# Performance work log

Measured on AMD Instinct MI355X. Metric: run time of the kernel, lower is better.

## Reference

```python
import jax, jax.numpy as jnp
import numpy as np

EMB = 128  # embedding_size hard-coded in source
NW = 8192  # weak samples
NS = 8192  # strong samples
FD = 1024  # encoder input feature dim
QN = 1024  # queue max_size
C = 80     # num classes (COCO-style WSOD)


def setup_inputs() -> dict:
    key = jax.random.key(0)
    ks = jax.random.split(key, 9)
    return {
        "feats_strong": jax.random.normal(ks[0], (NS, FD), jnp.float32),
        "feats_weak": jax.random.normal(ks[1], (NW, FD), jnp.float32),
        "strong_labels": jax.random.randint(ks[2], (NS,), 0, C, jnp.int64),
        "weak_labels": jax.random.randint(ks[3], (NW,), 0, C, jnp.int64),
        "Wq": jax.random.normal(ks[4], (FD, EMB), jnp.float32) * (FD ** -0.5),
        "bq": jax.random.normal(ks[5], (EMB,), jnp.float32) * 0.01,
        "Wk": jax.random.normal(ks[6], (FD, EMB), jnp.float32) * (FD ** -0.5),
        "bk": jax.random.normal(ks[7], (EMB,), jnp.float32) * 0.01,
        "queue": jax.random.normal(ks[8], (QN, EMB), jnp.float32),
    }


def reference(feats_strong, feats_weak, strong_labels, weak_labels, Wq, bq, Wk, bk, queue):
    # Encoders applied to all samples at once (original loops one-by-one).
    q_all = feats_weak @ Wq + bq            # [NW, EMB]
    k_all = feats_strong @ Wk + bk          # [NS, EMB]
    k_all = jax.lax.stop_gradient(k_all)    # k = k.detach() in source

    w, s = weak_labels, strong_labels
    eq_ws = w[:, None] == s[None, :]                      # [NW, NS] weak-vs-strong label match
    cnt = eq_ws.astype(jnp.int32).sum(1)                  # num_strong per weak sample
    valid = cnt > 0                                       # `if weak_label in strong_labels`

    # rank of i among weak indices with the same label (position in torch.where output)
    eq_ww = (w[:, None] == w[None, :]).astype(jnp.int32)
    rank = jnp.tril(eq_ww, -1).sum(1)                     # [NW]
    sel = rank % jnp.maximum(cnt, 1)                      # `% num_strong`

    # occurrence rank of each strong index within its label group
    eq_ss = (s[:, None] == s[None, :]).astype(jnp.int32)
    occ = jnp.tril(eq_ss, -1).sum(1)                      # [NS]

    # index_strong[i] = sel[i]-th strong index whose label == w[i]
    M = eq_ws & (occ[None, :] == sel[:, None])            # [NW, NS]
    idx = jnp.argmax(M, axis=1)                           # [NW]

    q = q_all                                             # [NW, EMB]
    k = k_all[idx]                                        # [NW, EMB]

    l_pos = jnp.sum(q * k, axis=-1, keepdims=True)        # bmm([N,1,E],[N,E,1]) -> [N,1]
    l_neg = q @ queue.reshape(EMB, -1)                    # queue.view(EMB, -1): row-major reshape
    logits = jnp.concatenate([l_pos, l_neg], axis=1)      # [NW, 1+QN]

    # CrossEntropy with target 0 on each valid row, mean over valid rows
    ce = -jax.nn.log_softmax(logits, axis=-1)[:, 0]
    m = valid.astype(logits.dtype)
    loss = jnp.sum(ce * m) / jnp.maximum(m.sum(), 1.0)
    return loss
```

## Files before the change

### kernel.cpp

```cpp
#include <hip/hip_runtime.h>
#include <hip/hip_bf16.h>

#define NW   8192
#define NS   8192
#define FD   1024
#define EMB  128
#define QN   1024
#define NC   80

typedef unsigned short ushort_t;
typedef unsigned int   uint_t;
typedef __attribute__((ext_vector_type(8))) short short8;
typedef __attribute__((ext_vector_type(4))) float f32x4;

#define OFF_Q      0u
#define OFF_K      1048576u
#define OFF_WTQ    2097152u
#define OFF_WTK    2129920u
#define OFF_HIST   2752512u
#define OFF_RANK   2752640u
#define OFF_CNT    2760832u
#define OFF_BHS    2785408u
#define OFF_BHW    2787968u
#define OFF_ACC    2790528u
#define OFF_QT     2790532u
#define OFF_TABLE  3000000u

__device__ __forceinline__ ushort_t f2bf(float f) {
    uint_t u = __float_as_uint(f);
    u = (u + 0x7fffu + ((u >> 16) & 1u)) >> 16;
    return (ushort_t)u;
}
__device__ __forceinline__ uint_t pack2(float a, float b) {
    return (uint_t)f2bf(a) | ((uint_t)f2bf(b) << 16);
}

#define GLOAD_LDS16(gp, lp)                                                     \
    __builtin_amdgcn_global_load_lds(                                           \
        (const __attribute__((address_space(1))) void*)(gp),                    \
        (__attribute__((address_space(3))) void*)(lp), 16, 0, 0)

__global__ __launch_bounds__(256) void cvtbh_k(const float* __restrict__ Wq,
                                               const float* __restrict__ Wk,
                                               const float* __restrict__ queue,
                                               const int* __restrict__ s_lab,
                                               const int* __restrict__ w_lab,
                                               ushort_t* __restrict__ Wtq,
                                               ushort_t* __restrict__ Wtk,
                                               ushort_t* __restrict__ Qt,
                                               int* __restrict__ bhs,
                                               int* __restrict__ bhw,
                                               float* __restrict__ accum,
                                               int* __restrict__ counter) {
    int bx = blockIdx.x;
    int t = threadIdx.x;
    if (bx >= 384) {
        __shared__ int h[NC];
        int b2 = bx - 384, z = b2 >> 5, cb = b2 & 31;
        const int* lab = z ? w_lab : s_lab;
        int* bh = z ? bhw : bhs;
        if (t < NC) h[t] = 0;
        __syncthreads();
        atomicAdd(&h[lab[cb * 256 + t]], 1);
        __syncthreads();
        if (t < NC) bh[cb * NC + t] = h[t];
        return;
    }
    __shared__ float tile[32][33];
    int z = bx >> 7, flat = bx & 127;
    if (z == 0 && flat == 0) {
        if (t < 2) accum[t] = 0.0f;
        if (t == 2) *counter = 0;
    }
    const float* in; ushort_t* out; int r0, c0, C;
    if (z < 2) { in = z ? Wk : Wq; out = z ? Wtk : Wtq; C = 128;
                 r0 = (flat >> 2) * 32; c0 = (flat & 3) * 32; }
    else       { in = queue; out = Qt; C = 1024;
                 r0 = (flat & 3) * 32; c0 = (flat >> 2) * 32; }
    int i = t >> 3, j0 = (t & 7) * 4;
    float4 v = *(const float4*)(in + (size_t)(r0 + i) * C + c0 + j0);
    tile[i][j0] = v.x; tile[i][j0 + 1] = v.y; tile[i][j0 + 2] = v.z; tile[i][j0 + 3] = v.w;
    __syncthreads();
    uint2 pk;
    pk.x = pack2(tile[j0][i], tile[j0 + 1][i]);
    pk.y = pack2(tile[j0 + 2][i], tile[j0 + 3][i]);
    size_t oaddr;
    int k0 = r0 + j0, n = c0 + i;
    if (z < 2) {
        oaddr = (size_t)(k0 >> 6) * 8192 + (size_t)((k0 >> 3) & 7) * 1024
              + (size_t)n * 8 + (k0 & 7);
    } else {
        int c = k0 >> 3;
        oaddr = ((size_t)n * 16 + (c ^ (n & 15))) * 8 + (k0 & 7);
    }
    *(uint2*)(out + oaddr) = pk;
}

__global__ __launch_bounds__(256) void enc_mfma_k(const float* __restrict__ A0,
                                                  const float* __restrict__ A1,
                                                  const ushort_t* __restrict__ Wt0,
                                                  const ushort_t* __restrict__ Wt1,
                                                  const float* __restrict__ b0_,
                                                  const float* __restrict__ b1_,
                                                  float* __restrict__ out0,
                                                  float* __restrict__ out1,
                                                  const int* __restrict__ s_lab,
                                                  const int* __restrict__ w_lab,
                                                  const int* __restrict__ bhs,
                                                  const int* __restrict__ bhw,
                                                  int* __restrict__ table,
                                                  int* __restrict__ rank,
                                                  int* __restrict__ hist) {
    __shared__ __align__(16) char smem[73728];

    int bx = blockIdx.x;
    int t = threadIdx.x;

    if (bx < 64) {
        int* ll = (int*)smem;
        int b2 = bx, z = b2 >> 5, cb = b2 & 31;
        const int* lab = z ? w_lab : s_lab;
        const int* bh = z ? bhw : bhs;
        int j = cb * 256 + t;
        int c = lab[j];
        ll[t] = c;
        __syncthreads();
        int r = 0;
        for (int b = 0; b < cb; b++) r += bh[b * NC + c];
        for (int jj = 0; jj < t; jj++) r += (ll[jj] == c) ? 1 : 0;
        if (z) rank[j] = r;
        else   table[c * 8192 + r] = j;
        if (b2 == 0 && t < 128) {
            int h = 0;
            if (t < NC)
                for (int b = 0; b < 32; b++) h += bhs[b * NC + t];
            hist[t] = h;
        }
        return;
    }

    int bxg = bx - 64;
    int which = bxg >> 8;
    int mtile = bxg & 255;
    const float*    A    = which ? A1 : A0;
    const ushort_t* Wt   = which ? Wt1 : Wt0;
    const float*    bias = which ? b1_ : b0_;
    float*          out  = which ? out1 : out0;
    int row0 = mtile * 32;

    int wv = t >> 6, ln = t & 63;
    int wm = wv >> 1, wn = wv & 1;
    int lane15 = ln & 15, kg = ln >> 4;

    int ar0 = wv * 8 + (ln >> 4);
    int ar1 = ar0 + 4;
    const float* gA0 = A + (size_t)(row0 + ar0) * FD + (((ln & 15) ^ (ar0 & 15))) * 4;
    const float* gA1 = A + (size_t)(row0 + ar1) * FD + (((ln & 15) ^ (ar1 & 15))) * 4;
    const ushort_t* gB = Wt + (size_t)wv * 2048 + ln * 8;

    f32x4 acc[4];
#pragma unroll
    for (int nt = 0; nt < 4; nt++) acc[nt] = (f32x4){0.f, 0.f, 0.f, 0.f};

#define STAGE(BUF, KB)                                                           \
    { char* sb = smem + (BUF) * 24576;                                           \
      GLOAD_LDS16(gA0 + (size_t)(KB) * 64, sb + wv * 2048);                      \
      GLOAD_LDS16(gA1 + (size_t)(KB) * 64, sb + wv * 2048 + 1024);               \
      const ushort_t* gb = gB + (size_t)(KB) * 8192;                             \
      char* bb = sb + 8192 + wv * 4096;                                          \
      GLOAD_LDS16(gb,        bb);                                                \
      GLOAD_LDS16(gb + 512,  bb + 1024);                                         \
      GLOAD_LDS16(gb + 1024, bb + 2048);                                         \
      GLOAD_LDS16(gb + 1536, bb + 3072); }

#define K2_ITER(KB, CURB, STB, VMSTR)                                            \
    { asm volatile("s_waitcnt vmcnt(" VMSTR ")" ::: "memory");                   \
      __builtin_amdgcn_s_barrier();                                              \
      __builtin_amdgcn_sched_barrier(0);                                         \
      if ((KB) < 14) STAGE(STB, (KB) + 2)                                        \
      { char* lb = smem + (CURB) * 24576;                                        \
        _Pragma("unroll")                                                        \
        for (int ks = 0; ks < 2; ks++) {                                         \
            int r_l = wm * 16 + lane15;                                          \
            int c0 = ks * 8 + kg * 2;                                            \
            float4 alo = *(const float4*)(lb + ((size_t)r_l * 16 + ((c0)     ^ (r_l & 15))) * 16); \
            float4 ahi = *(const float4*)(lb + ((size_t)r_l * 16 + ((c0 + 1) ^ (r_l & 15))) * 16); \
            uint4 pk;                                                            \
            pk.x = pack2(alo.x, alo.y); pk.y = pack2(alo.z, alo.w);              \
            pk.z = pack2(ahi.x, ahi.y); pk.w = pack2(ahi.z, ahi.w);              \
            short8 af = __builtin_bit_cast(short8, pk);                          \
            int kgg = ks * 4 + kg;                                               \
            _Pragma("unroll")                                                    \
            for (int nt = 0; nt < 4; nt++) {                                     \
                uint4 bv = *(const uint4*)(lb + 8192 +                           \
                            ((size_t)kgg * 128 + wn * 64 + nt * 16 + lane15) * 16); \
                acc[nt] = __builtin_amdgcn_mfma_f32_16x16x32_bf16(               \
                    af, __builtin_bit_cast(short8, bv), acc[nt], 0, 0, 0);       \
            }                                                                    \
        } }                                                                      \
    }

    STAGE(0, 0)
    STAGE(1, 1)
#pragma unroll 1
    for (int kb3 = 0; kb3 < 15; kb3 += 3) {
        K2_ITER(kb3 + 0, 0, 2, "6")
        K2_ITER(kb3 + 1, 1, 0, "6")
        K2_ITER(kb3 + 2, 2, 1, "6")
    }
    K2_ITER(15, 0, 0, "0")
#undef K2_ITER
#undef STAGE

#pragma unroll
    for (int nt = 0; nt < 4; nt++) {
        int col = wn * 64 + nt * 16 + lane15;
        float bv = bias[col];
        int rbase = row0 + wm * 16 + kg * 4;
#pragma unroll
        for (int j = 0; j < 4; j++)
            out[(size_t)(rbase + j) * EMB + col] = acc[nt][j] + bv;
    }
}

__global__ __launch_bounds__(256) void ce_mfma_k(const float* __restrict__ q,
                                                 const float* __restrict__ k,
                                                 const ushort_t* __restrict__ Qt,
                                                 const int* __restrict__ rank,
                                                 const int* __restrict__ table,
                                                 const int* __restrict__ w,
                                                 const int* __restrict__ hist,
                                                 float* __restrict__ accum,
                                                 int* __restrict__ counter,
                                                 float* __restrict__ outp) {
    __shared__ int   idx_lds[16];
    __shared__ float lpos_lds[16];
    __shared__ float mg[4][16][2];
    int t = threadIdx.x;
    int r0 = blockIdx.x * 16;

    if (t < 16) {
        int i = r0 + t;
        int c = w[i];
        int cc = hist[c];
        idx_lds[t] = (cc > 0) ? table[c * 8192 + (rank[i] % cc)] : 0;
    }
    __syncthreads();

    {
        int rr = t >> 4;
        int o = (t & 15) * 8;
        const float4* qa = (const float4*)(q + (size_t)(r0 + rr) * EMB + o);
        const float4* ka = (const float4*)(k + (size_t)idx_lds[rr] * EMB + o);
        float4 a0 = qa[0], b0 = ka[0], a1 = qa[1], b1 = ka[1];
        float s = a0.x * b0.x + a0.y * b0.y + a0.z * b0.z + a0.w * b0.w
                + a1.x * b1.x + a1.y * b1.y + a1.z * b1.z + a1.w * b1.w;
        s += __shfl_xor(s, 1); s += __shfl_xor(s, 2);
        s += __shfl_xor(s, 4); s += __shfl_xor(s, 8);
        if ((t & 15) == 0) lpos_lds[rr] = s;
    }

    int wv = t >> 6, ln = t & 63;
    int lane15 = ln & 15, kg = ln >> 4;

    short8 afr[4];
#pragma unroll
    for (int ks = 0; ks < 4; ks++) {
        const float4* p = (const float4*)(q + (size_t)(r0 + lane15) * EMB + ks * 32 + kg * 8);
        float4 a = p[0], b = p[1];
        uint4 pk;
        pk.x = pack2(a.x, a.y); pk.y = pack2(a.z, a.w);
        pk.z = pack2(b.x, b.y); pk.w = pack2(b.z, b.w);
        afr[ks] = __builtin_bit_cast(short8, pk);
    }

    f32x4 acc[16];
#pragma unroll
    for (int nc = 0; nc < 16; nc++) acc[nc] = (f32x4){0.f, 0.f, 0.f, 0.f};

#pragma unroll
    for (int nc = 0; nc < 16; nc++) {
        int n_g = nc * 64 + wv * 16 + lane15;
        const ushort_t* bp = Qt + (size_t)n_g * 128;
#pragma unroll
        for (int ks = 0; ks < 4; ks++) {
            int c = ks * 4 + kg;
            uint4 bb = *(const uint4*)(bp + (size_t)(c ^ lane15) * 8);
            acc[nc] = __builtin_amdgcn_mfma_f32_16x16x32_bf16(
                afr[ks], __builtin_bit_cast(short8, bb), acc[nc], 0, 0, 0);
        }
    }

#pragma unroll
    for (int j = 0; j < 4; j++) {
        float mx = -1e30f;
#pragma unroll
        for (int nc = 0; nc < 16; nc++) mx = fmaxf(mx, acc[nc][j]);
        mx = fmaxf(mx, __shfl_xor(mx, 1));
        mx = fmaxf(mx, __shfl_xor(mx, 2));
        mx = fmaxf(mx, __shfl_xor(mx, 4));
        mx = fmaxf(mx, __shfl_xor(mx, 8));
        float s = 0.f;
#pragma unroll
        for (int nc = 0; nc < 16; nc++) s += __expf(acc[nc][j] - mx);
        s += __shfl_xor(s, 1);
        s += __shfl_xor(s, 2);
        s += __shfl_xor(s, 4);
        s += __shfl_xor(s, 8);
        if (lane15 == 0) {
            mg[wv][kg * 4 + j][0] = mx;
            mg[wv][kg * 4 + j][1] = s;
        }
    }
    __syncthreads();
    if (wv == 0) {
        float cv = 0.f, cc = 0.f;
        if (t < 16) {
            int i = r0 + t;
            float m0 = mg[0][t][0], l0 = mg[0][t][1];
            float m1 = mg[1][t][0], l1 = mg[1][t][1];
            float m2 = mg[2][t][0], l2 = mg[2][t][1];
            float m3 = mg[3][t][0], l3 = mg[3][t][1];
            float lp = lpos_lds[t];
            float m = fmaxf(fmaxf(fmaxf(m0, m1), fmaxf(m2, m3)), lp);
            float l = l0 * __expf(m0 - m) + l1 * __expf(m1 - m)
                    + l2 * __expf(m2 - m) + l3 * __expf(m3 - m) + __expf(lp - m);
            float ce = -(lp - m - __logf(l));
            if (hist[w[i]] > 0) { cv = ce; cc = 1.f; }
        }
        cv += __shfl_xor(cv, 1);  cc += __shfl_xor(cc, 1);
        cv += __shfl_xor(cv, 2);  cc += __shfl_xor(cc, 2);
        cv += __shfl_xor(cv, 4);  cc += __shfl_xor(cc, 4);
        cv += __shfl_xor(cv, 8);  cc += __shfl_xor(cc, 8);
        if (t == 0) {
            atomicAdd(&accum[0], cv);
            atomicAdd(&accum[1], cc);
            __threadfence();
            int done = atomicAdd(counter, 1);
            if (done == 511) {
                float s = atomicAdd(&accum[0], 0.0f);
                float c = atomicAdd(&accum[1], 0.0f);
                outp[0] = s / fmaxf(c, 1.0f);
            }
        }
    }
}

extern "C" void kernel_launch(void* const* d_in, const int* in_sizes, int n_in,
                              void* d_out, int out_size, void* d_ws, size_t ws_size,
                              hipStream_t stream) {
    const float* feats_strong = (const float*)d_in[0];
    const float* feats_weak   = (const float*)d_in[1];
    const int*   s_lab        = (const int*)d_in[2];
    const int*   w_lab        = (const int*)d_in[3];
    const float* Wq           = (const float*)d_in[4];
    const float* bq           = (const float*)d_in[5];
    const float* Wk           = (const float*)d_in[6];
    const float* bk           = (const float*)d_in[7];
    const float* queue        = (const float*)d_in[8];

    float*    wsf = (float*)d_ws;
    int*      wsi = (int*)d_ws;

    float*    q_g   = wsf + OFF_Q;
    float*    k_g   = wsf + OFF_K;
    int*      table = wsi + OFF_TABLE;
    ushort_t* Wtq   = (ushort_t*)(wsi + OFF_WTQ);
    ushort_t* Wtk   = (ushort_t*)(wsi + OFF_WTK);
    int*      hist  = wsi + OFF_HIST;
    int*      rank  = wsi + OFF_RANK;
    int*      cnt   = wsi + OFF_CNT;
    int*      bhs   = wsi + OFF_BHS;
    int*      bhw   = wsi + OFF_BHW;
    float*    accum = wsf + OFF_ACC;
    ushort_t* Qt    = (ushort_t*)(wsi + OFF_QT);

    cvtbh_k<<<448, 256, 0, stream>>>(Wq, Wk, queue, s_lab, w_lab,
                                     Wtq, Wtk, Qt, bhs, bhw, accum, cnt);
    enc_mfma_k<<<576, 256, 0, stream>>>(feats_weak, feats_strong, Wtq, Wtk, bq, bk, q_g, k_g,
                                        s_lab, w_lab, bhs, bhw, table, rank, hist);
    ce_mfma_k<<<512, 256, 0, stream>>>(q_g, k_g, Qt, rank, table, w_lab, hist,
                                       accum, cnt, (float*)d_out);
}
```

Measured before the change: 163.0 us.

## Split CE kernel across 8 waves with double-buffered B loads and separate finalize

```diff
diff --git a/kernel.cpp b/kernel.cpp
--- a/kernel.cpp
+++ b/kernel.cpp
@@ -20,6 +20,7 @@
 #define OFF_HIST   2752512u
 #define OFF_RANK   2752640u
 #define OFF_CNT    2760832u
+#define OFF_PART   2760960u
 #define OFF_BHS    2785408u
 #define OFF_BHW    2787968u
 #define OFF_ACC    2790528u
@@ -223,19 +224,17 @@
     }
 }
 
-__global__ __launch_bounds__(256) void ce_mfma_k(const float* __restrict__ q,
-                                                 const float* __restrict__ k,
-                                                 const ushort_t* __restrict__ Qt,
-                                                 const int* __restrict__ rank,
-                                                 const int* __restrict__ table,
-                                                 const int* __restrict__ w,
-                                                 const int* __restrict__ hist,
-                                                 float* __restrict__ accum,
-                                                 int* __restrict__ counter,
-                                                 float* __restrict__ outp) {
+__global__ __launch_bounds__(512, 4) void ce_mfma_k(const float* __restrict__ q,
+                                                    const float* __restrict__ k,
+                                                    const ushort_t* __restrict__ Qt,
+                                                    const int* __restrict__ rank,
+                                                    const int* __restrict__ table,
+                                                    const int* __restrict__ w,
+                                                    const int* __restrict__ hist,
+                                                    float* __restrict__ part) {
     __shared__ int   idx_lds[16];
     __shared__ float lpos_lds[16];
-    __shared__ float mg[4][16][2];
+    __shared__ float mg[8][16][2];
     int t = threadIdx.x;
     int r0 = blockIdx.x * 16;
 
@@ -247,7 +246,7 @@
     }
     __syncthreads();
 
-    {
+    if (t < 256) {
         int rr = t >> 4;
         int o = (t & 15) * 8;
         const float4* qa = (const float4*)(q + (size_t)(r0 + rr) * EMB + o);
@@ -261,6 +260,7 @@
     }
 
     int wv = t >> 6, ln = t & 63;
+    int wgrp = wv >> 2, wq = wv & 3;
     int lane15 = ln & 15, kg = ln >> 4;
 
     short8 afr[4];
@@ -274,35 +274,48 @@
         afr[ks] = __builtin_bit_cast(short8, pk);
     }
 
-    f32x4 acc[16];
-#pragma unroll
-    for (int nc = 0; nc < 16; nc++) acc[nc] = (f32x4){0.f, 0.f, 0.f, 0.f};
-
-#pragma unroll
-    for (int nc = 0; nc < 16; nc++) {
-        int n_g = nc * 64 + wv * 16 + lane15;
-        const ushort_t* bp = Qt + (size_t)n_g * 128;
-#pragma unroll
-        for (int ks = 0; ks < 4; ks++) {
-            int c = ks * 4 + kg;
-            uint4 bb = *(const uint4*)(bp + (size_t)(c ^ lane15) * 8);
-            acc[nc] = __builtin_amdgcn_mfma_f32_16x16x32_bf16(
-                afr[ks], __builtin_bit_cast(short8, bb), acc[nc], 0, 0, 0);
-        }
-    }
+    f32x4 acc[8];
+#pragma unroll
+    for (int nc = 0; nc < 8; nc++) acc[nc] = (f32x4){0.f, 0.f, 0.f, 0.f};
+
+#define LOADB(DST, NCI)                                                          \
+    { int n_g = ((wgrp * 8 + (NCI)) * 64) + wq * 16 + lane15;                    \
+      const ushort_t* bp = Qt + (size_t)n_g * 128;                               \
+      _Pragma("unroll")                                                          \
+      for (int ks = 0; ks < 4; ks++)                                             \
+          DST[ks] = *(const uint4*)(bp + (size_t)(((ks * 4 + kg) ^ lane15)) * 8); }
+
+#define DO_MFMA(NC, B)                                                           \
+    { _Pragma("unroll")                                                          \
+      for (int ks = 0; ks < 4; ks++)                                             \
+          acc[NC] = __builtin_amdgcn_mfma_f32_16x16x32_bf16(                     \
+              afr[ks], __builtin_bit_cast(short8, (B)[ks]), acc[NC], 0, 0, 0); }
+
+    uint4 b0[4], b1[4];
+    LOADB(b0, 0)
+    LOADB(b1, 1)  DO_MFMA(0, b0)
+    LOADB(b0, 2)  DO_MFMA(1, b1)
+    LOADB(b1, 3)  DO_MFMA(2, b0)
+    LOADB(b0, 4)  DO_MFMA(3, b1)
+    LOADB(b1, 5)  DO_MFMA(4, b0)
+    LOADB(b0, 6)  DO_MFMA(5, b1)
+    LOADB(b1, 7)  DO_MFMA(6, b0)
+                  DO_MFMA(7, b1)
+#undef LOADB
+#undef DO_MFMA
 
 #pragma unroll
     for (int j = 0; j < 4; j++) {
         float mx = -1e30f;
 #pragma unroll
-        for (int nc = 0; nc < 16; nc++) mx = fmaxf(mx, acc[nc][j]);
+        for (int nc = 0; nc < 8; nc++) mx = fmaxf(mx, acc[nc][j]);
         mx = fmaxf(mx, __shfl_xor(mx, 1));
         mx = fmaxf(mx, __shfl_xor(mx, 2));
         mx = fmaxf(mx, __shfl_xor(mx, 4));
         mx = fmaxf(mx, __shfl_xor(mx, 8));
         float s = 0.f;
 #pragma unroll
-        for (int nc = 0; nc < 16; nc++) s += __expf(acc[nc][j] - mx);
+        for (int nc = 0; nc < 8; nc++) s += __expf(acc[nc][j] - mx);
         s += __shfl_xor(s, 1);
         s += __shfl_xor(s, 2);
         s += __shfl_xor(s, 4);
@@ -313,36 +326,51 @@
         }
     }
     __syncthreads();
-    if (wv == 0) {
+    if (t < 16) {
+        int i = r0 + t;
+        float lp = lpos_lds[t];
+        float m = lp;
+#pragma unroll
+        for (int v = 0; v < 8; v++) m = fmaxf(m, mg[v][t][0]);
+        float l = __expf(lp - m);
+#pragma unroll
+        for (int v = 0; v < 8; v++) l += mg[v][t][1] * __expf(mg[v][t][0] - m);
+        float ce = -(lp - m - __logf(l));
         float cv = 0.f, cc = 0.f;
-        if (t < 16) {
-            int i = r0 + t;
-            float m0 = mg[0][t][0], l0 = mg[0][t][1];
-            float m1 = mg[1][t][0], l1 = mg[1][t][1];
-            float m2 = mg[2][t][0], l2 = mg[2][t][1];
-            float m3 = mg[3][t][0], l3 = mg[3][t][1];
-            float lp = lpos_lds[t];
-            float m = fmaxf(fmaxf(fmaxf(m0, m1), fmaxf(m2, m3)), lp);
-            float l = l0 * __expf(m0 - m) + l1 * __expf(m1 - m)
-                    + l2 * __expf(m2 - m) + l3 * __expf(m3 - m) + __expf(lp - m);
-            float ce = -(lp - m - __logf(l));
-            if (hist[w[i]] > 0) { cv = ce; cc = 1.f; }
-        }
+        if (hist[w[i]] > 0) { cv = ce; cc = 1.f; }
         cv += __shfl_xor(cv, 1);  cc += __shfl_xor(cc, 1);
         cv += __shfl_xor(cv, 2);  cc += __shfl_xor(cc, 2);
         cv += __shfl_xor(cv, 4);  cc += __shfl_xor(cc, 4);
         cv += __shfl_xor(cv, 8);  cc += __shfl_xor(cc, 8);
         if (t == 0) {
-            atomicAdd(&accum[0], cv);
-            atomicAdd(&accum[1], cc);
-            __threadfence();
-            int done = atomicAdd(counter, 1);
-            if (done == 511) {
-                float s = atomicAdd(&accum[0], 0.0f);
-                float c = atomicAdd(&accum[1], 0.0f);
-                outp[0] = s / fmaxf(c, 1.0f);
-            }
+            float2* pp = (float2*)part;
+            pp[blockIdx.x] = make_float2(cv, cc);
         }
+    }
+}
+
+__global__ __launch_bounds__(256) void fin_k(const float* __restrict__ part,
+                                             float* __restrict__ outp) {
+    int t = threadIdx.x;
+    const float2* pp = (const float2*)part;
+    float cv = 0.f, cc = 0.f;
+    for (int i = t; i < 512; i += 256) {
+        float2 p = pp[i];
+        cv += p.x; cc += p.y;
+    }
+    cv += __shfl_xor(cv, 1);   cc += __shfl_xor(cc, 1);
+    cv += __shfl_xor(cv, 2);   cc += __shfl_xor(cc, 2);
+    cv += __shfl_xor(cv, 4);   cc += __shfl_xor(cc, 4);
+    cv += __shfl_xor(cv, 8);   cc += __shfl_xor(cc, 8);
+    cv += __shfl_xor(cv, 16);  cc += __shfl_xor(cc, 16);
+    cv += __shfl_xor(cv, 32);  cc += __shfl_xor(cc, 32);
+    __shared__ float sv[4], sc[4];
+    if ((t & 63) == 0) { sv[t >> 6] = cv; sc[t >> 6] = cc; }
+    __syncthreads();
+    if (t == 0) {
+        float s = sv[0] + sv[1] + sv[2] + sv[3];
+        float c = sc[0] + sc[1] + sc[2] + sc[3];
+        outp[0] = s / fmaxf(c, 1.0f);
     }
 }
 
@@ -373,12 +401,13 @@
     int*      bhs   = wsi + OFF_BHS;
     int*      bhw   = wsi + OFF_BHW;
     float*    accum = wsf + OFF_ACC;
+    float*    part  = wsf + OFF_PART;
     ushort_t* Qt    = (ushort_t*)(wsi + OFF_QT);
 
     cvtbh_k<<<448, 256, 0, stream>>>(Wq, Wk, queue, s_lab, w_lab,
                                      Wtq, Wtk, Qt, bhs, bhw, accum, cnt);
     enc_mfma_k<<<576, 256, 0, stream>>>(feats_weak, feats_strong, Wtq, Wtk, bq, bk, q_g, k_g,
                                         s_lab, w_lab, bhs, bhw, table, rank, hist);
-    ce_mfma_k<<<512, 256, 0, stream>>>(q_g, k_g, Qt, rank, table, w_lab, hist,
-                                       accum, cnt, (float*)d_out);
-}
+    ce_mfma_k<<<512, 512, 0, stream>>>(q_g, k_g, Qt, rank, table, w_lab, hist, part);
+    fin_k<<<1, 256, 0, stream>>>(part, (float*)d_out);
+}
```

Result: faster. 142.4 us (-12.7%).
